# Kernel tuning notes

Hardware: AMD Instinct MI355X
Metric: run time of the kernel (lower is better)

Reference implementation:

```python
import jax, jax.numpy as jnp
import numpy as np
import jax.lax as lax


def _log_bf_np(z, s2, s0):
    # Bayes factor per feature; s0 is the prior precision tau_0[l,k] (scalar)
    s0_inv = 1.0 / s0
    s2ps0inv = s2 + s0_inv
    return 0.5 * (jnp.log(s2) - jnp.log(s2ps0inv) + z ** 2 * (s0_inv / s2ps0inv))


def setup_inputs() -> dict:
    key = jax.random.key(0)
    ks = jax.random.split(key, 8)
    n, p, z, l = 1000, 50000, 20, 10
    data = jax.random.normal(ks[0], (n, p), jnp.float32)
    mean_z = jax.random.normal(ks[1], (n, z), jnp.float32)
    # factor second moment must be PSD with strictly positive diagonal (E_zzk > 0)
    mean_zz = (mean_z.T @ mean_z) / n + jnp.eye(z, dtype=jnp.float32)
    mean_w = jax.random.normal(ks[2], (l, z, p), jnp.float32) * 0.01
    var_w = jax.random.uniform(ks[3], (l, z), jnp.float32, minval=0.1, maxval=1.0)
    alpha = jax.random.uniform(ks[4], (l, z, p), jnp.float32)
    alpha = alpha / jnp.sum(alpha, axis=-1, keepdims=True)
    tau = jnp.asarray(1.5, jnp.float32)
    tau_0 = jax.random.uniform(ks[5], (l, z), jnp.float32, minval=0.5, maxval=2.0)
    pi = jax.random.uniform(ks[6], (z, p), jnp.float32, minval=0.5, maxval=1.5)
    pi = pi / jnp.sum(pi, axis=-1, keepdims=True)
    return {"data": data, "mean_z": mean_z, "mean_zz": mean_zz, "mean_w": mean_w,
            "var_w": var_w, "alpha": alpha, "tau": tau, "tau_0": tau_0, "pi": pi}


def reference(data, mean_z, mean_zz, mean_w, var_w, alpha, tau, tau_0, pi):
    """LoadingModel.update: sequential CAVI over factors (k) and single effects (l).
    mean_w/alpha: [l, z, p]; var_w/tau_0: [l, z]; pi: [z, p]; data: [n, p]; mean_z: [n, z].
    Returns updated (mean_w, var_w, alpha)."""
    l_dim, z_dim, p_dim = mean_w.shape
    # collapsed loading moments: W[k, :] = sum_l mean_w[l,k,:] * alpha[l,k,:]
    W = jnp.sum(mean_w * alpha, axis=0)            # [z, p]
    ZtX = mean_z.T @ data                           # [z, p] (precompute of mean_z[:,k] @ data)
    log_pi = jnp.log(pi)                            # [z, p]

    def factor_step(carry, kdx):
        W, mean_w, var_w, alpha = carry
        E_zzk = mean_zz[kdx, kdx]
        Wk = W[kdx]                                 # [p]
        # Wnk.T @ E_zpzk over j != k  ==  mean_zz[kdx] @ W - E_zzk * Wk (avoids the gather)
        RtZk = ZtX[kdx] - (mean_zz[kdx] @ W - E_zzk * Wk)   # [p]
        log_pi_k = log_pi[kdx]
        s2_s = 1.0 / (E_zzk * tau)
        zs_scale = jnp.sqrt(E_zzk * tau) / E_zzk

        def effect_step(Wk, xs):
            mw_l, a_l, t0_l = xs                    # [p], [p], scalar
            Wkl = Wk - mw_l * a_l                   # remove effect l from residual fit
            E_RtZk = RtZk - E_zzk * Wkl             # [p]
            var_new = jnp.reciprocal(tau * E_zzk + t0_l)   # scalar
            mean_new = tau * var_new * E_RtZk       # [p]
            Z_s = E_RtZk * zs_scale
            log_bf = _log_bf_np(Z_s, s2_s, t0_l)
            alpha_new = jax.nn.softmax(log_pi_k + log_bf)
            Wk_new = Wkl + mean_new * alpha_new
            return Wk_new, (mean_new, var_new, alpha_new)

        Wk_new, (mw_rows, vw_rows, a_rows) = lax.scan(
            effect_step, Wk, (mean_w[:, kdx, :], alpha[:, kdx, :], tau_0[:, kdx]))
        mean_w = mean_w.at[:, kdx, :].set(mw_rows)
        var_w = var_w.at[:, kdx].set(vw_rows)
        alpha = alpha.at[:, kdx, :].set(a_rows)
        W = W.at[kdx].set(Wk_new)
        return (W, mean_w, var_w, alpha), None

    (W, mean_w, var_w, alpha), _ = lax.scan(
        factor_step, (W, mean_w, var_w, alpha), jnp.arange(z_dim))
    return mean_w, var_w, alpha
```

## Files before the change

kernel.cpp:

```cpp
#include <hip/hip_runtime.h>
#include <stdint.h>


#define NTHREADS 256
#define NBLK 196
constexpr int N_DIM = 1000;
constexpr int P_DIM = 50000;
constexpr int Z_DIM = 20;
constexpr int L_DIM = 10;

using u64 = unsigned long long;

__device__ __forceinline__ float wred_max(float v) {
#pragma unroll
  for (int m = 32; m; m >>= 1) v = fmaxf(v, __shfl_xor(v, m, 64));
  return v;
}
__device__ __forceinline__ float wred_sum(float v) {
#pragma unroll
  for (int m = 32; m; m >>= 1) v += __shfl_xor(v, m, 64);
  return v;
}

__global__ __launch_bounds__(NTHREADS) void loading_model_kernel(
    const float* __restrict__ data,
    const float* __restrict__ mean_z,
    const float* __restrict__ mean_zz,
    const float* __restrict__ mean_w_in,
    const float* __restrict__ alpha_in,
    const float* __restrict__ tau_p,
    const float* __restrict__ tau0,
    const float* __restrict__ pi,
    float* __restrict__ out_mw,
    float* __restrict__ out_vw,
    float* __restrict__ out_alpha,
    u64* __restrict__ ws)
{
  const int tid  = threadIdx.x;
  const int blk  = blockIdx.x;
  const int gid  = blk * NTHREADS + tid;
  const bool active = (gid < P_DIM);
  const int lane = tid & 63;
  const int wid  = tid >> 6;
  const float tau = tau_p[0];

  __shared__ float lds_wmax[4];
  __shared__ float lds_wsum[4];
  __shared__ float lds_lse;

  if (blk == 0 && tid < L_DIM * Z_DIM) {
    int k = tid % Z_DIM;
    float E = mean_zz[k * Z_DIM + k];
    out_vw[tid] = 1.0f / (tau * E + tau0[tid]);
  }

  float ztx[Z_DIM];
#pragma unroll
  for (int k = 0; k < Z_DIM; k++) ztx[k] = 0.f;
  {
    const float* dcol = data + gid;
#pragma unroll 8
    for (int n = 0; n < N_DIM; n++) {
      float d = active ? dcol[(size_t)n * P_DIM] : 0.f;
#pragma unroll
      for (int k = 0; k < Z_DIM; k++) ztx[k] += mean_z[n * Z_DIM + k] * d;
    }
  }

  float W[Z_DIM];
#pragma unroll
  for (int j = 0; j < Z_DIM; j++) W[j] = 0.f;
  for (int l = 0; l < L_DIM; l++) {
#pragma unroll
    for (int j = 0; j < Z_DIM; j++) {
      if (active) {
        size_t idx = ((size_t)(l * Z_DIM + j)) * P_DIM + gid;
        W[j] += mean_w_in[idx] * alpha_in[idx];
      }
    }
  }

  u64* slots = ws;

  float pival = active ? pi[gid] : 1.0f;
  float mw = 0.f, av = 0.f;
  if (active) { mw = mean_w_in[gid]; av = alpha_in[gid]; }

  const float E0    = mean_zz[0];
  const float ktau0 = tau * E0;
  float cs2   = 1.0f / ktau0;
  float czsc2 = tau / E0;
  float nc0, nc1, nmnc;
  {
    const float t0    = tau0[0];
    const float s0inv = 1.0f / t0;
    const float s2p   = cs2 + s0inv;
    nc0  = 0.5f * (__logf(cs2) - __logf(s2p));
    nc1  = 0.5f * czsc2 * (s0inv / s2p);
    nmnc = tau / (ktau0 + t0);
  }

#pragma unroll
  for (int k = 0; k < Z_DIM; k++) {
    const float E    = mean_zz[k * Z_DIM + k];
    const float ktau = tau * E;

    float acc = 0.f;
#pragma unroll
    for (int j = 0; j < Z_DIM; j++) acc += mean_zz[k * Z_DIM + j] * W[j];
    const float RtZk = ztx[k] - (acc - E * W[k]);
    const float lpk  = active ? __logf(pival) : -INFINITY;
    if (k + 1 < Z_DIM && active) pival = pi[(size_t)(k + 1) * P_DIM + gid];

    float Wk = W[k];
    for (int l = 0; l < L_DIM; l++) {
      const float c0  = nc0;
      const float c1  = nc1;
      const float mnc = nmnc;

      const float Wkl = Wk - mw * av;
      const float E_R = RtZk - E * Wkl;
      const float mean_new = mnc * E_R;
      float logit = lpk + c0 + c1 * E_R * E_R;
      if (!active) logit = -INFINITY;

      const size_t oidx = ((size_t)(l * Z_DIM + k)) * P_DIM + gid;
      if (active) out_mw[oidx] = mean_new;

      float wmax = wred_max(logit);
      float ew   = active ? __expf(logit - wmax) : 0.f;
      float wsum = wred_sum(ew);
      if (lane == 0) { lds_wmax[wid] = wmax; lds_wsum[wid] = wsum; }
      __syncthreads();

      const int s   = k * L_DIM + l + 1;
      const int buf = s & 1;
      if (tid == 0) {
        float m0 = lds_wmax[0], m1 = lds_wmax[1];
        float m2 = lds_wmax[2], m3 = lds_wmax[3];
        float M4 = fmaxf(fmaxf(m0, m1), fmaxf(m2, m3));
        float S4 = __expf(m0 - M4) * lds_wsum[0] + __expf(m1 - M4) * lds_wsum[1]
                 + __expf(m2 - M4) * lds_wsum[2] + __expf(m3 - M4) * lds_wsum[3];
        float lse_b = M4 + __logf(S4);
        __hip_atomic_store(&slots[buf * NBLK + blk],
                           (((u64)(unsigned)s) << 32) | (u64)__float_as_uint(lse_b),
                           __ATOMIC_RELAXED, __HIP_MEMORY_SCOPE_AGENT);
      }

      float mw_n = 0.f, av_n = 0.f;
      {
        int ln = l + 1, kn = k;
        if (ln == L_DIM) { ln = 0; kn = k + 1; }
        if (kn < Z_DIM) {
          if (active) {
            size_t idx2 = ((size_t)(ln * Z_DIM + kn)) * P_DIM + gid;
            mw_n = mean_w_in[idx2];
            av_n = alpha_in[idx2];
          }
          if (ln == 0) {
            const float En = mean_zz[kn * Z_DIM + kn];
            const float kt = tau * En;
            cs2   = 1.0f / kt;
            czsc2 = tau / En;
          }
          const float t0n   = tau0[ln * Z_DIM + kn];
          const float s0inv = 1.0f / t0n;
          const float s2p   = cs2 + s0inv;
          nc0  = 0.5f * (__logf(cs2) - __logf(s2p));
          nc1  = 0.5f * czsc2 * (s0inv / s2p);
          nmnc = (ln == 0) ? tau / (tau * mean_zz[kn * Z_DIM + kn] + t0n)
                           : tau / (ktau + t0n);
        }
      }

      if (wid == 0) {
        u64 raw[4];
        bool need[4];
#pragma unroll
        for (int q = 0; q < 4; q++) need[q] = (lane + (q << 6)) < NBLK;
        bool pend = true;
        while (pend) {
#pragma unroll
          for (int q = 0; q < 4; q++) {
            int j = lane + (q << 6);
            if (need[q])
              raw[q] = __hip_atomic_load(&slots[buf * NBLK + j],
                                         __ATOMIC_RELAXED, __HIP_MEMORY_SCOPE_AGENT);
          }
          pend = false;
#pragma unroll
          for (int q = 0; q < 4; q++) {
            if (need[q]) {
              if ((unsigned)(raw[q] >> 32) == (unsigned)s) need[q] = false;
              else pend = true;
            }
          }
        }
        float m = -INFINITY;
#pragma unroll
        for (int q = 0; q < 4; q++) {
          int j = lane + (q << 6);
          if (j < NBLK) m = fmaxf(m, __uint_as_float((unsigned)raw[q]));
        }
        float M = wred_max(m);
        float ps = 0.f;
#pragma unroll
        for (int q = 0; q < 4; q++) {
          int j = lane + (q << 6);
          if (j < NBLK) ps += __expf(__uint_as_float((unsigned)raw[q]) - M);
        }
        float S = wred_sum(ps);
        if (lane == 0) lds_lse = M + __logf(S);
      }
      __syncthreads();

      const float LSEt = lds_lse;
      const float alpha_new = active ? __expf(logit - LSEt) : 0.f;
      Wk = Wkl + mean_new * alpha_new;
      if (active) out_alpha[oidx] = alpha_new;
      mw = mw_n;
      av = av_n;
    }
    W[k] = Wk;
  }
}

extern "C" void kernel_launch(void* const* d_in, const int* in_sizes, int n_in,
                              void* d_out, int out_size, void* d_ws, size_t ws_size,
                              hipStream_t stream) {
  const float* data    = (const float*)d_in[0];
  const float* mean_z  = (const float*)d_in[1];
  const float* mean_zz = (const float*)d_in[2];
  const float* mean_w  = (const float*)d_in[3];
  const float* alpha   = (const float*)d_in[5];
  const float* tau     = (const float*)d_in[6];
  const float* tau0    = (const float*)d_in[7];
  const float* pi      = (const float*)d_in[8];

  float* out_mw    = (float*)d_out;
  float* out_vw    = out_mw + (size_t)L_DIM * Z_DIM * P_DIM;
  float* out_alpha = out_vw + (size_t)L_DIM * Z_DIM;
  u64*   ws        = (u64*)d_ws;

  hipMemsetAsync(d_ws, 0, 2 * NBLK * sizeof(u64), stream);

  void* args[] = {(void*)&data, (void*)&mean_z, (void*)&mean_zz, (void*)&mean_w,
                  (void*)&alpha, (void*)&tau, (void*)&tau0, (void*)&pi,
                  (void*)&out_mw, (void*)&out_vw, (void*)&out_alpha, (void*)&ws};
  hipLaunchCooperativeKernel((void*)loading_model_kernel, dim3(NBLK),
                             dim3(NTHREADS), args, 0, stream);
}
```

Before: 1.333 ms.

## Split precompute into separate kernel and shrink cooperative grid to 49 large blocks

Moves the ZtX matmul and W collapse into a separate wide kernel that stashes results in the output buffers. The sequential CAVI kernel then runs 49 blocks of 1024 threads, so each grid-wide log-sum-exp exchange polls only 49 slots with one load per lane. This targets the per-step cross-block synchronization cost. It adds an extra kernel launch and a global round-trip for the stash, and reusing output buffers as scratch risks races between blocks.

```diff
diff --git a/kernel.cpp b/kernel.cpp
--- a/kernel.cpp
+++ b/kernel.cpp
@@ -2,13 +2,21 @@
 #include <stdint.h>
 
 
-#define NTHREADS 256
-#define NBLK 196
+#define NTA 128
+#define NBLKA 392
+#define NT_B 1024
+#define NBLK_B 49
+#define NWAVE_B (NT_B / 64)
+#define PSTRIDE 50176
+
 constexpr int N_DIM = 1000;
 constexpr int P_DIM = 50000;
 constexpr int Z_DIM = 20;
 constexpr int L_DIM = 10;
 
+static_assert(NTA * NBLKA == PSTRIDE, "phase A covers PSTRIDE columns");
+static_assert(NT_B * NBLK_B == PSTRIDE, "phase B covers PSTRIDE columns");
+
 using u64 = unsigned long long;
 
 __device__ __forceinline__ float wred_max(float v) {
@@ -22,7 +30,7 @@
   return v;
 }
 
-__global__ __launch_bounds__(NTHREADS) void loading_model_kernel(
+__global__ __launch_bounds__(NTA) void precompute_kernel(
     const float* __restrict__ data,
     const float* __restrict__ mean_z,
     const float* __restrict__ mean_zz,
@@ -30,28 +38,16 @@
     const float* __restrict__ alpha_in,
     const float* __restrict__ tau_p,
     const float* __restrict__ tau0,
-    const float* __restrict__ pi,
-    float* __restrict__ out_mw,
-    float* __restrict__ out_vw,
-    float* __restrict__ out_alpha,
-    u64* __restrict__ ws)
+    float* __restrict__ ztx_stash,
+    float* __restrict__ W_stash,
+    float* __restrict__ out_vw)
 {
-  const int tid  = threadIdx.x;
-  const int blk  = blockIdx.x;
-  const int gid  = blk * NTHREADS + tid;
+  const int gid = blockIdx.x * NTA + threadIdx.x;
   const bool active = (gid < P_DIM);
-  const int lane = tid & 63;
-  const int wid  = tid >> 6;
-  const float tau = tau_p[0];
-
-  __shared__ float lds_wmax[4];
-  __shared__ float lds_wsum[4];
-  __shared__ float lds_lse;
-
-  if (blk == 0 && tid < L_DIM * Z_DIM) {
-    int k = tid % Z_DIM;
-    float E = mean_zz[k * Z_DIM + k];
-    out_vw[tid] = 1.0f / (tau * E + tau0[tid]);
+
+  if (gid < L_DIM * Z_DIM) {
+    int k = gid % Z_DIM;
+    out_vw[gid] = 1.0f / (tau_p[0] * mean_zz[k * Z_DIM + k] + tau0[gid]);
   }
 
   float ztx[Z_DIM];
@@ -66,6 +62,8 @@
       for (int k = 0; k < Z_DIM; k++) ztx[k] += mean_z[n * Z_DIM + k] * d;
     }
   }
+#pragma unroll
+  for (int k = 0; k < Z_DIM; k++) ztx_stash[(size_t)k * PSTRIDE + gid] = ztx[k];
 
   float W[Z_DIM];
 #pragma unroll
@@ -79,8 +77,40 @@
       }
     }
   }
-
-  u64* slots = ws;
+#pragma unroll
+  for (int j = 0; j < Z_DIM; j++) W_stash[(size_t)j * PSTRIDE + gid] = W[j];
+}
+
+__global__ __launch_bounds__(NT_B) void loading_model_seq(
+    const float* __restrict__ mean_zz,
+    const float* __restrict__ mean_w_in,
+    const float* __restrict__ alpha_in,
+    const float* __restrict__ tau_p,
+    const float* __restrict__ tau0,
+    const float* __restrict__ pi,
+    const float* __restrict__ ztx_stash,
+    const float* __restrict__ W_stash,
+    float* __restrict__ out_mw,
+    float* __restrict__ out_alpha,
+    u64* __restrict__ slots)
+{
+  const int tid  = threadIdx.x;
+  const int blk  = blockIdx.x;
+  const int gid  = blk * NT_B + tid;
+  const bool active = (gid < P_DIM);
+  const int lane = tid & 63;
+  const int wid  = tid >> 6;
+  const float tau = tau_p[0];
+
+  __shared__ float lds_wmax[NWAVE_B];
+  __shared__ float lds_wsum[NWAVE_B];
+  __shared__ float lds_lse;
+
+  float ztx[Z_DIM], W[Z_DIM];
+#pragma unroll
+  for (int k = 0; k < Z_DIM; k++) ztx[k] = ztx_stash[(size_t)k * PSTRIDE + gid];
+#pragma unroll
+  for (int j = 0; j < Z_DIM; j++) W[j] = W_stash[(size_t)j * PSTRIDE + gid];
 
   float pival = active ? pi[gid] : 1.0f;
   float mw = 0.f, av = 0.f;
@@ -135,16 +165,21 @@
 
       const int s   = k * L_DIM + l + 1;
       const int buf = s & 1;
-      if (tid == 0) {
-        float m0 = lds_wmax[0], m1 = lds_wmax[1];
-        float m2 = lds_wmax[2], m3 = lds_wmax[3];
-        float M4 = fmaxf(fmaxf(m0, m1), fmaxf(m2, m3));
-        float S4 = __expf(m0 - M4) * lds_wsum[0] + __expf(m1 - M4) * lds_wsum[1]
-                 + __expf(m2 - M4) * lds_wsum[2] + __expf(m3 - M4) * lds_wsum[3];
-        float lse_b = M4 + __logf(S4);
-        __hip_atomic_store(&slots[buf * NBLK + blk],
-                           (((u64)(unsigned)s) << 32) | (u64)__float_as_uint(lse_b),
-                           __ATOMIC_RELAXED, __HIP_MEMORY_SCOPE_AGENT);
+      if (wid == 0) {
+        const int li = lane & (NWAVE_B - 1);
+        const bool val = (lane < NWAVE_B);
+        float m  = lds_wmax[li];
+        float sv = lds_wsum[li];
+        m  = val ? m  : -INFINITY;
+        sv = val ? sv : 0.f;
+        float M = wred_max(m);
+        float S = wred_sum(val ? __expf(m - M) * sv : 0.f);
+        if (lane == 0) {
+          float lse_b = M + __logf(S);
+          __hip_atomic_store(&slots[buf * NBLK_B + blk],
+                             (((u64)(unsigned)s) << 32) | (u64)__float_as_uint(lse_b),
+                             __ATOMIC_RELAXED, __HIP_MEMORY_SCOPE_AGENT);
+        }
       }
 
       float mw_n = 0.f, av_n = 0.f;
@@ -174,42 +209,17 @@
       }
 
       if (wid == 0) {
-        u64 raw[4];
-        bool need[4];
-#pragma unroll
-        for (int q = 0; q < 4; q++) need[q] = (lane + (q << 6)) < NBLK;
-        bool pend = true;
-        while (pend) {
-#pragma unroll
-          for (int q = 0; q < 4; q++) {
-            int j = lane + (q << 6);
-            if (need[q])
-              raw[q] = __hip_atomic_load(&slots[buf * NBLK + j],
-                                         __ATOMIC_RELAXED, __HIP_MEMORY_SCOPE_AGENT);
-          }
-          pend = false;
-#pragma unroll
-          for (int q = 0; q < 4; q++) {
-            if (need[q]) {
-              if ((unsigned)(raw[q] >> 32) == (unsigned)s) need[q] = false;
-              else pend = true;
-            }
-          }
+        bool need = (lane < NBLK_B);
+        u64 raw = 0;
+        while (need) {
+          raw = __hip_atomic_load(&slots[buf * NBLK_B + lane],
+                                  __ATOMIC_RELAXED, __HIP_MEMORY_SCOPE_AGENT);
+          if ((unsigned)(raw >> 32) == (unsigned)s) need = false;
         }
-        float m = -INFINITY;
-#pragma unroll
-        for (int q = 0; q < 4; q++) {
-          int j = lane + (q << 6);
-          if (j < NBLK) m = fmaxf(m, __uint_as_float((unsigned)raw[q]));
-        }
-        float M = wred_max(m);
-        float ps = 0.f;
-#pragma unroll
-        for (int q = 0; q < 4; q++) {
-          int j = lane + (q << 6);
-          if (j < NBLK) ps += __expf(__uint_as_float((unsigned)raw[q]) - M);
-        }
-        float S = wred_sum(ps);
+        float bl = (lane < NBLK_B) ? __uint_as_float((unsigned)raw) : -INFINITY;
+        float M  = wred_max(bl);
+        float ps = (lane < NBLK_B) ? __expf(bl - M) : 0.f;
+        float S  = wred_sum(ps);
         if (lane == 0) lds_lse = M + __logf(S);
       }
       __syncthreads();
@@ -242,11 +252,19 @@
   float* out_alpha = out_vw + (size_t)L_DIM * Z_DIM;
   u64*   ws        = (u64*)d_ws;
 
-  hipMemsetAsync(d_ws, 0, 2 * NBLK * sizeof(u64), stream);
-
-  void* args[] = {(void*)&data, (void*)&mean_z, (void*)&mean_zz, (void*)&mean_w,
-                  (void*)&alpha, (void*)&tau, (void*)&tau0, (void*)&pi,
-                  (void*)&out_mw, (void*)&out_vw, (void*)&out_alpha, (void*)&ws};
-  hipLaunchCooperativeKernel((void*)loading_model_kernel, dim3(NBLK),
-                             dim3(NTHREADS), args, 0, stream);
-}
+  float* ztx_stash = out_mw;
+  float* W_stash   = out_alpha;
+
+  hipMemsetAsync(d_ws, 0, 2 * NBLK_B * sizeof(u64), stream);
+
+  hipLaunchKernelGGL(precompute_kernel, dim3(NBLKA), dim3(NTA), 0, stream,
+                     data, mean_z, mean_zz, mean_w, alpha, tau, tau0,
+                     ztx_stash, W_stash, out_vw);
+
+  void* args[] = {(void*)&mean_zz, (void*)&mean_w, (void*)&alpha,
+                  (void*)&tau, (void*)&tau0, (void*)&pi,
+                  (void*)&ztx_stash, (void*)&W_stash,
+                  (void*)&out_mw, (void*)&out_alpha, (void*)&ws};
+  hipLaunchCooperativeKernel((void*)loading_model_seq, dim3(NBLK_B),
+                             dim3(NT_B), args, 0, stream);
+}
```

Result: slower. 1.383 ms (+3.7%).
